# Kernel tuning notes

Measured on AMD Instinct MI355X. Metric: run time of the kernel, lower is better.

Reference implementation:

```python
import jax, jax.numpy as jnp
import numpy as np
import math

B, L, D = 4, 4096, 1024
D_EMB, D_HID = 3, 16


def make_pos_emb(emb_dim, seq_len):
    # Complex exponential positional embeddings (non-trainable), shape (1, seq_len, emb_dim)
    t = np.linspace(0.0, 1.0, seq_len, dtype=np.float32)[None, :, None]
    bands = (emb_dim - 1) // 2
    t_res = np.linspace(0.0, seq_len - 1, seq_len, dtype=np.float32)[None, :, None]
    w = 2.0 * math.pi * t_res / seq_len
    f = np.linspace(0.0001, max(bands - 1, 0), bands, dtype=np.float32)[None, None]
    z = np.exp(-1j * (f * w).astype(np.complex64))
    z = np.concatenate([t, z.real.astype(np.float32), z.imag.astype(np.float32)], axis=-1)
    return jnp.asarray(z)


def setup_inputs() -> dict:
    key = jax.random.key(0)
    ks = jax.random.split(key, 8)
    u = jax.random.normal(ks[0], (B, L, D), dtype=jnp.float32)
    z = make_pos_emb(D_EMB, L)  # (1, L, D_EMB)
    # filter MLP: Linear(d_emb, d_hidden) -> ReLU -> Linear(d_hidden, d_model)
    s1 = 1.0 / math.sqrt(D_EMB)
    w1 = jax.random.uniform(ks[1], (D_HID, D_EMB), jnp.float32, -s1, s1)
    b1 = jax.random.uniform(ks[2], (D_HID,), jnp.float32, -s1, s1)
    s2 = 1.0 / math.sqrt(D_HID)
    w2 = jax.random.uniform(ks[3], (D, D_HID), jnp.float32, -s2, s2)
    b2 = jax.random.uniform(ks[4], (D,), jnp.float32, -s2, s2)
    # projection: Linear(d_model, d_model)
    sp = 1.0 / math.sqrt(D)
    pw = jax.random.uniform(ks[5], (D, D), jnp.float32, -sp, sp)
    pb = jax.random.uniform(ks[6], (D,), jnp.float32, -sp, sp)
    return {"u": u, "z": z, "w1": w1, "b1": b1, "w2": w2, "b2": b2, "pw": pw, "pb": pb}


def fft_conv(u_bdl, k_dl):
    # u_bdl: (B, D, L), k_dl: (1, D, L) or (D, L)
    seqlen = u_bdl.shape[-1]
    fft_size = 2 * seqlen
    k_f = jnp.fft.rfft(k_dl, n=fft_size) / fft_size
    u_f = jnp.fft.rfft(u_bdl, n=fft_size)
    y = jnp.fft.irfft(u_f * k_f, n=fft_size, norm="forward")[..., :seqlen]
    return y


def reference(u, z, w1, b1, w2, b2, pw, pb):
    seqlen = u.shape[1]
    pe = z[:, :seqlen]  # (1, L, D_EMB)
    h = jax.nn.relu(jnp.einsum("ble,he->blh", pe, w1) + b1)
    filt = jnp.einsum("blh,dh->bld", h, w2) + b2  # (1, L, D)
    filt = jnp.transpose(filt, (0, 2, 1))  # (1, D, L)
    u_conv = fft_conv(jnp.transpose(u, (0, 2, 1)), filt)  # (B, D, L)
    u_conv = jnp.transpose(u_conv, (0, 2, 1)).astype(u.dtype)  # (B, L, D)
    u_proj = jnp.einsum("bld,od->blo", u, pw) + pb
    return u_conv * u_proj + u
```

## Files before the change

kernel.cpp:

```cpp
#include <hip/hip_runtime.h>
#include <hip/hip_bf16.h>

#define SEQL 4096
#define DCH  1024
#define BATCH 4

typedef __attribute__((ext_vector_type(2))) float cf;
__device__ __forceinline__ cf mkc(float x, float y){ cf r; r.x = x; r.y = y; return r; }
__device__ __forceinline__ cf cadd(cf a, cf b){ return a + b; }
__device__ __forceinline__ cf csub(cf a, cf b){ return a - b; }
__device__ __forceinline__ cf cmul(cf a, cf b){ return a.xx * b + mkc(-a.y, a.y) * b.yx; }
__device__ __forceinline__ cf cconjf(cf a){ return mkc(a.x, -a.y); }
__device__ __forceinline__ cf addi(cf a, cf b){ return a + mkc(-b.y, b.x); }
__device__ __forceinline__ cf subi(cf a, cf b){ return a - mkc(-b.y, b.x); }
__device__ __forceinline__ int phi(int c){ return c ^ ((c >> 4) & 15); }
__device__ __forceinline__ int drev(int i){
    return ((i>>10)&3) | (((i>>8)&3)<<2) | (((i>>6)&3)<<4)
         | (((i>>4)&3)<<6) | (((i>>2)&3)<<8) | ((i&3)<<10);
}

__device__ __forceinline__ cf W1c(int j){
    const float cs[4] = {1.f, 0.92387953f, 0.70710678f, 0.38268343f};
    const float sn[4] = {0.f, -0.38268343f, -0.70710678f, -0.92387953f};
    return mkc(cs[j], sn[j]);
}
__device__ __forceinline__ cf W2c(int j){
    const float cs[4] = {1.f, 0.70710678f, 0.f, -0.70710678f};
    const float sn[4] = {0.f, -0.70710678f, -1.f, -0.70710678f};
    return mkc(cs[j], sn[j]);
}
__device__ __forceinline__ cf W3c(int j){
    const float cs[4] = {1.f, 0.38268343f, -0.70710678f, -0.92387953f};
    const float sn[4] = {0.f, -0.92387953f, -0.70710678f, 0.38268343f};
    return mkc(cs[j], sn[j]);
}

__device__ __forceinline__ unsigned pack2bf(float a, float b){
    unsigned r;
    asm("v_cvt_pk_bf16_f32 %0, %1, %2" : "=v"(r) : "v"(a), "v"(b));
    return r;
}
__device__ __forceinline__ float bflo(unsigned u){ return __uint_as_float(u << 16); }
__device__ __forceinline__ float bfhi(unsigned u){ return __uint_as_float(u & 0xffff0000u); }

__device__ __forceinline__ void gload16(const void* g, void* l){
    __builtin_amdgcn_global_load_lds((const __attribute__((address_space(1))) void*)g,
                                     (__attribute__((address_space(3))) void*)l, 16, 0, 0);
}

__global__ __launch_bounds__(256) void prep_kernel(
        cf* __restrict__ tw4, cf* __restrict__ tw8, unsigned* __restrict__ idxt,
        const float* __restrict__ z, const float* __restrict__ w1,
        const float* __restrict__ b1, float* __restrict__ h,
        const float* __restrict__ pw, unsigned short* __restrict__ pwb) {
    const int blk = blockIdx.x;
    if (blk < 16) {
        int i = blk * 256 + threadIdx.x;
        const double TWO_PI = 6.283185307179586476925286766559;
        double a4 = -TWO_PI * (double)i / 4096.0;
        double a8 = -TWO_PI * (double)i / 8192.0;
        tw4[i] = mkc((float)cos(a4), (float)sin(a4));
        tw8[i] = mkc((float)cos(a8), (float)sin(a8));
    } else if (blk < 32) {
        int l = (blk - 16) * 256 + threadIdx.x;
        float pe0 = z[l * 3 + 0], pe1 = z[l * 3 + 1], pe2 = z[l * 3 + 2];
#pragma unroll
        for (int j = 0; j < 16; ++j) {
            float v = pe0 * w1[j * 3 + 0] + pe1 * w1[j * 3 + 1] + pe2 * w1[j * 3 + 2] + b1[j];
            h[l * 16 + j] = v > 0.f ? v : 0.f;
        }
    } else if (blk < 40) {
        int k = (blk - 32) * 256 + threadIdx.x;
        unsigned sk  = (unsigned)phi(drev(k));
        unsigned skk = (unsigned)phi(drev(4096 - k));
        idxt[k] = sk | (skk << 16);
    } else if (pwb) {
        int t = (blk - 40) * 256 + threadIdx.x;
        float4 a = *(const float4*)&pw[(size_t)t * 8];
        float4 b = *(const float4*)&pw[(size_t)t * 8 + 4];
        uint4 o;
        o.x = pack2bf(a.x, a.y); o.y = pack2bf(a.z, a.w);
        o.z = pack2bf(b.x, b.y); o.w = pack2bf(b.z, b.w);
        *(uint4*)&pwb[(size_t)t * 8] = o;
    }
}

__global__ __launch_bounds__(256) void transpose_kernel(
        const float* __restrict__ u, unsigned* __restrict__ utb,
        unsigned short* __restrict__ ub) {
    __shared__ float tile[32][33];
    int b = blockIdx.z;
    int l0 = blockIdx.x * 32;
    int d0 = blockIdx.y * 32;
    int tx = threadIdx.x, ty = threadIdx.y;
    const float* up = u + (size_t)b * SEQL * DCH;
    unsigned short* ubp = ub ? ub + (size_t)b * SEQL * DCH : (unsigned short*)0;
#pragma unroll
    for (int i = 0; i < 32; i += 8) {
        size_t idx = (size_t)(l0 + ty + i) * DCH + d0 + tx;
        float v = up[idx];
        tile[ty + i][tx] = v;
        if (ub) ubp[idx] = (unsigned short)pack2bf(v, v);
    }
    __syncthreads();
    unsigned* utp = utb + (size_t)b * DCH * (SEQL / 2);
    int t  = ty * 32 + tx;
    int dl = t >> 4;
    int lp = t & 15;
#pragma unroll
    for (int p = 0; p < 2; ++p) {
        int dd = dl + p * 16;
        unsigned v = pack2bf(tile[2 * lp][dd], tile[2 * lp + 1][dd]);
        utp[(size_t)(d0 + dd) * (SEQL / 2) + (l0 >> 1) + lp] = v;
    }
}

__device__ void dif_mid_and_chunk(cf* lds, const cf* __restrict__ tw){
    const int tid = threadIdx.x;
#pragma unroll
    for (int p = 1; p < 4; ++p) {
        const int lm = 10 - 2*p;
        const int m  = 1 << lm;
        const int step = 1024 >> lm;
#pragma unroll
        for (int it = 0; it < 4; ++it) {
            int j = tid + (it << 8);
            int k = j & (m-1);
            int g = j >> lm;
            int i0 = (g << (lm+2)) + k;
            cf x0 = lds[phi(i0)];
            cf x1 = lds[phi(i0+m)];
            cf x2 = lds[phi(i0+2*m)];
            cf x3 = lds[phi(i0+3*m)];
            cf b0 = cadd(x0,x2), b1 = csub(x0,x2);
            cf b2 = cadd(x1,x3), b3 = csub(x1,x3);
            cf u0 = cadd(b0,b2);
            cf u2 = csub(b0,b2);
            cf u1 = subi(b1,b3);
            cf u3 = addi(b1,b3);
            int t1 = k*step;
            lds[phi(i0)]     = u0;
            lds[phi(i0+m)]   = cmul(u1, tw[t1]);
            lds[phi(i0+2*m)] = cmul(u2, tw[2*t1]);
            lds[phi(i0+3*m)] = cmul(u3, tw[3*t1]);
        }
        __syncthreads();
    }
    {
        const int b0 = tid << 4;
        const int xr = tid & 15;
        cf v[16];
#pragma unroll
        for (int j=0;j<16;++j) v[j] = lds[b0 + (j ^ xr)];
#pragma unroll
        for (int j=0;j<4;++j){
            cf x0=v[j], x1=v[j+4], x2=v[j+8], x3=v[j+12];
            cf b0v=cadd(x0,x2), b1=csub(x0,x2), b2=cadd(x1,x3), b3=csub(x1,x3);
            cf u0=cadd(b0v,b2), u2=csub(b0v,b2), u1=subi(b1,b3), u3=addi(b1,b3);
            v[j]    = u0;
            v[j+4]  = cmul(u1, W1c(j));
            v[j+8]  = cmul(u2, W2c(j));
            v[j+12] = cmul(u3, W3c(j));
        }
#pragma unroll
        for (int c=0;c<4;++c){
            cf x0=v[4*c], x1=v[4*c+1], x2=v[4*c+2], x3=v[4*c+3];
            cf b0v=cadd(x0,x2), b1=csub(x0,x2), b2=cadd(x1,x3), b3=csub(x1,x3);
            v[4*c]   = cadd(b0v,b2);
            v[4*c+1] = subi(b1,b3);
            v[4*c+2] = csub(b0v,b2);
            v[4*c+3] = addi(b1,b3);
        }
#pragma unroll
        for (int j=0;j<16;++j) lds[b0 + (j ^ xr)] = v[j];
        __syncthreads();
    }
}

__device__ void dit_chunk_and_mid(cf* lds, const cf* __restrict__ tw){
    const int tid = threadIdx.x;
    {
        const int b0 = tid << 4;
        const int xr = tid & 15;
        cf v[16];
#pragma unroll
        for (int j=0;j<16;++j) v[j] = lds[b0 + (j ^ xr)];
#pragma unroll
        for (int c=0;c<4;++c){
            cf a0=v[4*c], a1=v[4*c+1], a2=v[4*c+2], a3=v[4*c+3];
            cf b0v=cadd(a0,a2), b1=csub(a0,a2), b2=cadd(a1,a3), b3=csub(a1,a3);
            v[4*c]   = cadd(b0v,b2);
            v[4*c+1] = addi(b1,b3);
            v[4*c+2] = csub(b0v,b2);
            v[4*c+3] = subi(b1,b3);
        }
#pragma unroll
        for (int j=0;j<4;++j){
            cf a0=v[j];
            cf a1=cmul(v[j+4],  cconjf(W1c(j)));
            cf a2=cmul(v[j+8],  cconjf(W2c(j)));
            cf a3=cmul(v[j+12], cconjf(W3c(j)));
            cf b0v=cadd(a0,a2), b1=csub(a0,a2), b2=cadd(a1,a3), b3=csub(a1,a3);
            v[j]    = cadd(b0v,b2);
            v[j+4]  = addi(b1,b3);
            v[j+8]  = csub(b0v,b2);
            v[j+12] = subi(b1,b3);
        }
#pragma unroll
        for (int j=0;j<16;++j) lds[b0 + (j ^ xr)] = v[j];
        __syncthreads();
    }
#pragma unroll
    for (int p = 0; p < 3; ++p) {
        const int lm = 4 + 2*p;
        const int m  = 1 << lm;
        const int step = 1024 >> lm;
#pragma unroll
        for (int it = 0; it < 4; ++it) {
            int j = tid + (it << 8);
            int k = j & (m-1);
            int g = j >> lm;
            int i0 = (g << (lm+2)) + k;
            int t1 = k*step;
            cf a0 = lds[phi(i0)];
            cf a1 = cmul(lds[phi(i0+m)],   cconjf(tw[t1]));
            cf a2 = cmul(lds[phi(i0+2*m)], cconjf(tw[2*t1]));
            cf a3 = cmul(lds[phi(i0+3*m)], cconjf(tw[3*t1]));
            cf b0=cadd(a0,a2), b1=csub(a0,a2), b2=cadd(a1,a3), b3=csub(a1,a3);
            lds[phi(i0)]     = cadd(b0,b2);
            lds[phi(i0+m)]   = addi(b1,b3);
            lds[phi(i0+2*m)] = csub(b0,b2);
            lds[phi(i0+3*m)] = subi(b1,b3);
        }
        __syncthreads();
    }
}

__global__ __launch_bounds__(256) void filt_fft_kernel(
        const float* __restrict__ h, const float* __restrict__ w2,
        const float* __restrict__ b2, const cf* __restrict__ tw4,
        const cf* __restrict__ tw8, cf* __restrict__ kfP,
        cf* __restrict__ kfP2, cf* __restrict__ kfQ) {
    __shared__ cf lds[4096];
    const int d = blockIdx.x;
    const int tid = threadIdx.x;
    float wv[16];
#pragma unroll
    for (int j = 0; j < 16; ++j) wv[j] = w2[d * 16 + j];
    const float bb = b2[d];
#pragma unroll
    for (int it = 0; it < 4; ++it) {
        int j = tid + (it << 8);
        const float* h0 = h + (size_t)(2*j) * 16;
        const float* h1 = h + (size_t)(2*(j+1024)) * 16;
        float f0 = bb, f1 = bb, f2 = bb, f3 = bb;
#pragma unroll
        for (int i = 0; i < 16; ++i) {
            f0 += h0[i] * wv[i];  f1 += h0[16+i] * wv[i];
            f2 += h1[i] * wv[i];  f3 += h1[16+i] * wv[i];
        }
        cf x0 = mkc(f0, f1), x1 = mkc(f2, f3);
        cf u0 = cadd(x0,x1);
        cf u2 = csub(x0,x1);
        cf u1 = subi(x0,x1);
        cf u3 = addi(x0,x1);
        lds[phi(j)]      = u0;
        lds[phi(j+1024)] = cmul(u1, tw4[j]);
        lds[phi(j+2048)] = cmul(u2, tw4[2*j]);
        lds[phi(j+3072)] = cmul(u3, tw4[3*j]);
    }
    __syncthreads();
    dif_mid_and_chunk(lds, tw4);
    const float s = 1.f / 8192.f;
    cf* Prow  = kfP  + (size_t)d * 2048;
    cf* P2row = kfP2 + (size_t)d * 2048;
    cf* Qrow  = kfQ  + (size_t)d * 2048;
    const int lane  = tid & 63;
    const int kbase = ((lane & 31) << 6) | ((lane >> 5) << 5) | ((tid >> 6) << 3);
#pragma unroll
    for (int it = 0; it < 8; ++it) {
        int k = kbase + it;
        if (k == 0) {
            cf c0 = lds[0];
            float H0 = (c0.x + c0.y) * s;
            float H4 = (c0.x - c0.y) * s;
            Prow[0]  = mkc(H0 + H4, H0 - H4);
            P2row[0] = mkc(H0 - H4, H0 + H4);
            cf c2 = lds[2];
            Qrow[0] = mkc(2.f * s * c2.x, 2.f * s * c2.y);
        } else {
            int kk = 4096 - k;
            cf ck  = lds[phi(drev(k))];
            cf ckk = lds[phi(drev(kk))];
            cf cc = cconjf(ckk);
            cf E  = (ck + cc) * 0.5f;
            cf Dd = csub(ck, cc);
            cf O  = mkc(Dd.y, -Dd.x) * 0.5f;
            cf wvv = tw8[k];
            cf Xk  = cadd(E, cmul(wvv, O));
            cf wp  = mkc(-wvv.x, wvv.y);
            cf Xkk = cadd(cconjf(E), cmul(wp, cconjf(O)));
            cf Hk  = Xk * s;
            cf Hkk = Xkk * s;
            float a = 1.f + wvv.y;
            float b = 1.f - wvv.y;
            cf Hkb = cconjf(Hkk);
            cf Hkc = cconjf(Hk);
            Prow[k]  = Hk * a + Hkb * b;
            P2row[k] = Hkk * a + Hkc * b;
            cf Qd = csub(Hk, Hkb);
            Qrow[k] = mkc(-Qd.y, Qd.x) * wvv.x;
        }
    }
}

__global__ __launch_bounds__(256) void conv_kernel(
        unsigned* __restrict__ utyb, const cf* __restrict__ tw4,
        const unsigned* __restrict__ idxt, const cf* __restrict__ kfP,
        const cf* __restrict__ kfP2, const cf* __restrict__ kfQ) {
    __shared__ cf lds[4096];
    const int row = blockIdx.x;
    const int d = row & (DCH - 1);
    const int tid = threadIdx.x;
    unsigned* rp = utyb + (size_t)row * (SEQL / 2);
#pragma unroll
    for (int it = 0; it < 4; ++it) {
        int j = tid + (it << 8);
        unsigned q0 = rp[j], q1 = rp[j + 1024];
        cf x0 = mkc(bflo(q0), bfhi(q0));
        cf x1 = mkc(bflo(q1), bfhi(q1));
        cf u0 = cadd(x0,x1);
        cf u2 = csub(x0,x1);
        cf u1 = subi(x0,x1);
        cf u3 = addi(x0,x1);
        lds[phi(j)]      = u0;
        lds[phi(j+1024)] = cmul(u1, tw4[j]);
        lds[phi(j+2048)] = cmul(u2, tw4[2*j]);
        lds[phi(j+3072)] = cmul(u3, tw4[3*j]);
    }
    __syncthreads();
    dif_mid_and_chunk(lds, tw4);
    const cf* Prow  = kfP  + (size_t)d * 2048;
    const cf* P2row = kfP2 + (size_t)d * 2048;
    const cf* Qrow  = kfQ  + (size_t)d * 2048;
    {
        const int lane  = tid & 63;
        const int kbase = ((lane & 31) << 6) | ((lane >> 5) << 5) | ((tid >> 6) << 3);
#pragma unroll
        for (int it = 0; it < 8; ++it) {
            int k = kbase + it;
            if (k == 0) {
                cf P0 = Prow[0], C0 = P2row[0], Q0 = Qrow[0];
                cf c0 = lds[0];
                lds[0] = P0 * c0.x + C0 * c0.y;
                cf c2 = lds[2];
                lds[2] = cmul(Q0, c2);
            } else {
                unsigned iv = idxt[k];
                int sk  = iv & 0xffff;
                int skk = iv >> 16;
                cf ck = lds[sk], ckk = lds[skk];
                cf Pv = Prow[k], P2v = P2row[k], Qv = Qrow[k];
                cf Zk  = cadd(cmul(Pv, ck),  cmul(Qv, cconjf(ckk)));
                cf Zkk = csub(cmul(P2v, ckk), cmul(cconjf(Qv), cconjf(ck)));
                lds[sk] = Zk; lds[skk] = Zkk;
            }
        }
    }
    __syncthreads();
    dit_chunk_and_mid(lds, tw4);
#pragma unroll
    for (int it = 0; it < 4; ++it) {
        int j = tid + (it << 8);
        cf a0 = lds[phi(j)];
        cf a1 = cmul(lds[phi(j+1024)], cconjf(tw4[j]));
        cf a2 = cmul(lds[phi(j+2048)], cconjf(tw4[2*j]));
        cf a3 = cmul(lds[phi(j+3072)], cconjf(tw4[3*j]));
        cf b0 = cadd(a0,a2), b1 = csub(a0,a2);
        cf b2 = cadd(a1,a3), b3 = csub(a1,a3);
        cf o0 = cadd(b0,b2);
        cf o1 = addi(b1,b3);
        rp[j]        = pack2bf(o0.x, o0.y);
        rp[j + 1024] = pack2bf(o1.x, o1.y);
    }
}

typedef __attribute__((ext_vector_type(8))) short short8;
typedef __attribute__((ext_vector_type(4))) float f32x4;

__global__ __launch_bounds__(512, 2) void gemm_mfma_v3(
        const unsigned short* __restrict__ ub, const unsigned short* __restrict__ pwb,
        const float* __restrict__ pb, const unsigned short* __restrict__ yb,
        float* __restrict__ out) {
    __shared__ char lds_raw[147456];
    float (*ysc)[132] = (float(*)[132])lds_raw;

    const int tid  = threadIdx.x;
    const int lane = tid & 63;
    const int wid  = tid >> 6;
    const int wr   = wid >> 1;
    const int wc   = wid & 1;
    const int m0   = blockIdx.x * 256;
    const int n0   = blockIdx.y * 128;

    f32x4 acc[4][4] = {};

#pragma unroll
    for (int tt = 0; tt < 2; ++tt) {
#pragma unroll
        for (int un = 0; un < 3; ++un) {
            const unsigned short* gs = (un == 2) ? pwb : ub;
            int growb = (un == 2) ? n0 : (m0 + un * 128);
#pragma unroll
            for (int j = 0; j < 2; ++j) {
                int rr = j * 64 + (tid >> 3);
                int ss = (tid & 7) ^ ((tid >> 3) & 7);
                gload16(gs + (size_t)(growb + rr) * 1024 + tt * 64 + ss * 8,
                        lds_raw + tt * 49152 + un * 16384 + rr * 128 + (tid & 7) * 16);
            }
        }
    }
    asm volatile("s_waitcnt vmcnt(6)" ::: "memory");
    __builtin_amdgcn_sched_barrier(0);
    __builtin_amdgcn_s_barrier();

    for (int t = 0; t < 16; ++t) {
        const int Ab  = (t % 3) * 49152;
        const int Bb  = Ab + 32768;
        const int sbB = ((t + 2) % 3) * 49152;
        const int kt2 = (t + 2) * 64;
#pragma unroll
        for (int q = 0; q < 4; ++q) {
            const int qr = q >> 1, qc = q & 1;
            short8 af[2][2], bfr[2][2];
#pragma unroll
            for (int f = 0; f < 2; ++f) {
                int arow = wr * 64 + qr * 32 + f * 16 + (lane & 15);
                int brow = wc * 64 + qc * 32 + f * 16 + (lane & 15);
#pragma unroll
                for (int kh = 0; kh < 2; ++kh) {
                    int ks = (lane >> 4) + 4 * kh;
                    af[f][kh]  = *(short8*)(lds_raw + Ab + arow * 128 + (ks ^ (arow & 7)) * 16);
                    bfr[f][kh] = *(short8*)(lds_raw + Bb + brow * 128 + (ks ^ (brow & 7)) * 16);
                }
            }
            if (q < 3 && t < 14) {
                const unsigned short* gs = (q == 2) ? pwb : ub;
                int growb = (q == 2) ? n0 : (m0 + q * 128);
#pragma unroll
                for (int j = 0; j < 2; ++j) {
                    int rr = j * 64 + (tid >> 3);
                    int ss = (tid & 7) ^ ((tid >> 3) & 7);
                    gload16(gs + (size_t)(growb + rr) * 1024 + kt2 + ss * 8,
                            lds_raw + sbB + q * 16384 + rr * 128 + (tid & 7) * 16);
                }
            }
            __builtin_amdgcn_s_barrier();
            asm volatile("s_waitcnt lgkmcnt(0)" ::: "memory");
            __builtin_amdgcn_sched_barrier(0);
            __builtin_amdgcn_s_setprio(1);
#pragma unroll
            for (int fa = 0; fa < 2; ++fa)
#pragma unroll
                for (int fb = 0; fb < 2; ++fb)
#pragma unroll
                    for (int kh = 0; kh < 2; ++kh)
                        acc[qr * 2 + fa][qc * 2 + fb] = __builtin_amdgcn_mfma_f32_16x16x32_bf16(
                            af[fa][kh], bfr[fb][kh], acc[qr * 2 + fa][qc * 2 + fb], 0, 0, 0);
            __builtin_amdgcn_s_setprio(0);
            if (q == 3) {
                if (t < 14)       asm volatile("s_waitcnt vmcnt(6)" ::: "memory");
                else if (t == 14) asm volatile("s_waitcnt vmcnt(0)" ::: "memory");
                __builtin_amdgcn_sched_barrier(0);
            }
            __builtin_amdgcn_s_barrier();
        }
    }

    __syncthreads();
    const int b  = m0 >> 12;
    const int l0 = m0 & (SEQL - 1);
    float pbv[4];
#pragma unroll
    for (int nf = 0; nf < 4; ++nf)
        pbv[nf] = pb[n0 + wc * 64 + nf * 16 + (lane & 15)];

    for (int c = 0; c < 2; ++c) {
        __syncthreads();
        {
            int dn = tid >> 2;
            int lq = tid & 3;
            const uint4* uptr = (const uint4*)(yb + (((size_t)(b * DCH + n0 + dn)) << 12) + l0 + c * 128);
#pragma unroll
            for (int jj = 0; jj < 4; ++jj) {
                uint4 w4 = uptr[lq * 4 + jj];
                int lb = (lq * 4 + jj) * 8;
                ysc[lb+0][dn] = bflo(w4.x); ysc[lb+1][dn] = bfhi(w4.x);
                ysc[lb+2][dn] = bflo(w4.y); ysc[lb+3][dn] = bfhi(w4.y);
                ysc[lb+4][dn] = bflo(w4.z); ysc[lb+5][dn] = bfhi(w4.z);
                ysc[lb+6][dn] = bflo(w4.w); ysc[lb+7][dn] = bfhi(w4.w);
            }
        }
        __syncthreads();
        if ((wr >> 1) == c) {
#pragma unroll
            for (int mf = 0; mf < 4; ++mf)
#pragma unroll
                for (int i = 0; i < 4; ++i) {
                    int lrow = (wr & 1) * 64 + mf * 16 + (lane >> 4) * 4 + i;
                    int m = m0 + c * 128 + lrow;
#pragma unroll
                    for (int nf = 0; nf < 4; ++nf) {
                        int nl = wc * 64 + nf * 16 + (lane & 15);
                        int n = n0 + nl;
                        float proj = acc[mf][nf][i] + pbv[nf];
                        float ures = __uint_as_float((unsigned)ub[(size_t)m * DCH + n] << 16);
                        out[(size_t)m * DCH + n] = ysc[lrow][nl] * proj + ures;
                    }
                }
        }
    }
}

__global__ __launch_bounds__(256, 3) void gemm_mfma_fb(
        const float* __restrict__ u, const float* __restrict__ pw,
        const float* __restrict__ pb, const unsigned short* __restrict__ yb,
        float* __restrict__ out) {
    __shared__ char lds_raw[34816];
    float (*ysc)[132] = (float(*)[132])lds_raw;
    const int tid  = threadIdx.x;
    const int lane = tid & 63;
    const int wid  = tid >> 6;
    const int wr   = wid >> 1;
    const int wc   = wid & 1;
    const int m0   = blockIdx.x * 128;
    const int n0   = blockIdx.y * 128;
    f32x4 acc[4][4] = {};
    float4 ra[4], rb[4];
    int s_row[4], s_f4[4];
#pragma unroll
    for (int j = 0; j < 4; ++j) {
        int idx = j * 256 + tid;
        s_row[j] = idx >> 3;
        s_f4[j]  = idx & 7;
    }
#define LOADT(kt)                                                                     \
    {                                                                                 \
        _Pragma("unroll")                                                             \
        for (int j = 0; j < 4; ++j) {                                                 \
            ra[j] = *(const float4*)&u [(size_t)(m0 + s_row[j]) * DCH + (kt) + s_f4[j] * 4]; \
            rb[j] = *(const float4*)&pw[(size_t)(n0 + s_row[j]) * DCH + (kt) + s_f4[j] * 4]; \
        }                                                                             \
    }
#define WRITET(base)                                                                  \
    {                                                                                 \
        _Pragma("unroll")                                                             \
        for (int j = 0; j < 4; ++j) {                                                 \
            int off = (base) + ((s_row[j] * 64 + s_f4[j] * 8) ^ ((s_row[j] & 3) << 4)); \
            uint2 pa, pbv2;                                                           \
            pa.x   = pack2bf(ra[j].x, ra[j].y);  pa.y   = pack2bf(ra[j].z, ra[j].w);  \
            pbv2.x = pack2bf(rb[j].x, rb[j].y);  pbv2.y = pack2bf(rb[j].z, rb[j].w);  \
            *(uint2*)(lds_raw + off)        = pa;                                     \
            *(uint2*)(lds_raw + off + 8192) = pbv2;                                   \
        }                                                                             \
    }
    LOADT(0);
    WRITET(0);
    LOADT(32);
    __syncthreads();
    for (int t = 0; t < 32; ++t) {
        const int cur = (t & 1) << 14;
        short8 af[4], bfr[4];
#pragma unroll
        for (int f = 0; f < 4; ++f) {
            int rowA = wr * 64 + f * 16 + (lane & 15);
            int rowB = wc * 64 + f * 16 + (lane & 15);
            int offA = cur + ((rowA * 64 + ((lane >> 4) * 16)) ^ ((rowA & 3) << 4));
            int offB = cur + 8192 + ((rowB * 64 + ((lane >> 4) * 16)) ^ ((rowB & 3) << 4));
            af[f]  = *(short8*)(lds_raw + offA);
            bfr[f] = *(short8*)(lds_raw + offB);
        }
        if (t < 31) WRITET(cur ^ 16384);
        if (t < 30) LOADT((t + 2) * 32);
#pragma unroll
        for (int mf = 0; mf < 4; ++mf)
#pragma unroll
            for (int nf = 0; nf < 4; ++nf)
                acc[mf][nf] = __builtin_amdgcn_mfma_f32_16x16x32_bf16(
                    af[mf], bfr[nf], acc[mf][nf], 0, 0, 0);
        __syncthreads();
    }
    const int b  = m0 >> 12;
    const int l0 = m0 & (SEQL - 1);
    float pbv[4];
#pragma unroll
    for (int nf = 0; nf < 4; ++nf)
        pbv[nf] = pb[n0 + wc * 64 + nf * 16 + (lane & 15)];
    for (int c = 0; c < 2; ++c) {
        __syncthreads();
#pragma unroll
        for (int j = 0; j < 4; ++j) {
            int idx = j * 256 + tid;
            int dn  = idx >> 3;
            int lg  = idx & 7;
            uint4 w4 = *(const uint4*)&yb[(((size_t)(b * DCH + n0 + dn)) << 12) + l0 + c * 64 + lg * 8];
            int lb = lg * 8;
            ysc[lb+0][dn] = bflo(w4.x); ysc[lb+1][dn] = bfhi(w4.x);
            ysc[lb+2][dn] = bflo(w4.y); ysc[lb+3][dn] = bfhi(w4.y);
            ysc[lb+4][dn] = bflo(w4.z); ysc[lb+5][dn] = bfhi(w4.z);
            ysc[lb+6][dn] = bflo(w4.w); ysc[lb+7][dn] = bfhi(w4.w);
        }
        __syncthreads();
        if (wr == c) {
#pragma unroll
            for (int mf = 0; mf < 4; ++mf)
#pragma unroll
                for (int i = 0; i < 4; ++i) {
                    int lrow = mf * 16 + (lane >> 4) * 4 + i;
                    int m = m0 + c * 64 + lrow;
#pragma unroll
                    for (int nf = 0; nf < 4; ++nf) {
                        int nl = wc * 64 + nf * 16 + (lane & 15);
                        int n = n0 + nl;
                        float proj = acc[mf][nf][i] + pbv[nf];
                        out[(size_t)m * DCH + n] = ysc[lrow][nl] * proj + u[(size_t)m * DCH + n];
                    }
                }
        }
    }
#undef LOADT
#undef WRITET
}

extern "C" void kernel_launch(void* const* d_in, const int* in_sizes, int n_in,
                              void* d_out, int out_size, void* d_ws, size_t ws_size,
                              hipStream_t stream) {
    const float* u  = (const float*)d_in[0];
    const float* z  = (const float*)d_in[1];
    const float* w1 = (const float*)d_in[2];
    const float* b1 = (const float*)d_in[3];
    const float* w2 = (const float*)d_in[4];
    const float* b2 = (const float*)d_in[5];
    const float* pw = (const float*)d_in[6];
    const float* pb = (const float*)d_in[7];
    float* out = (float*)d_out;

    float*    h    = (float*)d_ws;
    unsigned* utyb = (unsigned*)((char*)d_ws + 262144);

    cf* kfP  = (cf*)d_out;
    cf* kfP2 = (cf*)((char*)d_out + (16u << 20));
    cf* kfQ  = (cf*)((char*)d_out + (32u << 20));

    const size_t ub_off  = 262144 + (size_t)BATCH * DCH * (SEQL / 2) * sizeof(unsigned);
    const size_t pwb_off = ub_off + (size_t)BATCH * SEQL * DCH * sizeof(unsigned short);
    const size_t tw_off  = pwb_off + (size_t)DCH * DCH * sizeof(unsigned short);
    const size_t need    = tw_off + 2 * 4096 * sizeof(cf) + 2048 * sizeof(unsigned);
    const bool   big     = ws_size >= need;

    cf* tw4; unsigned* idxt;
    if (big) {
        tw4  = (cf*)((char*)d_ws + tw_off);
    } else {
        tw4  = (cf*)((char*)d_out + (56u << 20));
    }
    cf* tw8 = tw4 + 4096;
    idxt = (unsigned*)(tw8 + 4096);
    unsigned short* ub  = big ? (unsigned short*)((char*)d_ws + ub_off)  : (unsigned short*)0;
    unsigned short* pwb = big ? (unsigned short*)((char*)d_ws + pwb_off) : (unsigned short*)0;

    prep_kernel<<<dim3(big ? 552 : 40), dim3(256), 0, stream>>>(tw4, tw8, idxt, z, w1, b1, h, pw, pwb);
    transpose_kernel<<<dim3(SEQL / 32, DCH / 32, BATCH), dim3(32, 8), 0, stream>>>(u, utyb, ub);
    filt_fft_kernel<<<dim3(DCH), dim3(256), 0, stream>>>(h, w2, b2, tw4, tw8, kfP, kfP2, kfQ);
    conv_kernel<<<dim3(BATCH * DCH), dim3(256), 0, stream>>>(utyb, tw4, idxt, kfP, kfP2, kfQ);
    if (big)
        gemm_mfma_v3<<<dim3(64, 8), dim3(512), 0, stream>>>(ub, pwb, pb, (const unsigned short*)utyb, out);
    else
        gemm_mfma_fb<<<dim3(128, 8), dim3(256), 0, stream>>>(u, pw, pb, (const unsigned short*)utyb, out);
}
```

Measured before the change: 259.1 us.

## Run FFT conv and filter kernels with 512 threads and radix-4 stages

Doubles the block size of the filter FFT and convolution kernels from 256 to 512 threads. Each thread now does 2 instead of 4 radix-4 butterflies per stage. The in-register 16-point chunk is replaced by an extra LDS radix-4 stage plus an 8-element per-thread chunk. The aim is more parallelism per block and lower register pressure, so latency is hidden better. In exchange there is one more LDS pass and one more barrier per FFT direction.

```diff
diff --git a/kernel.cpp b/kernel.cpp
--- a/kernel.cpp
+++ b/kernel.cpp
@@ -17,22 +17,6 @@
 __device__ __forceinline__ int drev(int i){
     return ((i>>10)&3) | (((i>>8)&3)<<2) | (((i>>6)&3)<<4)
          | (((i>>4)&3)<<6) | (((i>>2)&3)<<8) | ((i&3)<<10);
-}
-
-__device__ __forceinline__ cf W1c(int j){
-    const float cs[4] = {1.f, 0.92387953f, 0.70710678f, 0.38268343f};
-    const float sn[4] = {0.f, -0.38268343f, -0.70710678f, -0.92387953f};
-    return mkc(cs[j], sn[j]);
-}
-__device__ __forceinline__ cf W2c(int j){
-    const float cs[4] = {1.f, 0.70710678f, 0.f, -0.70710678f};
-    const float sn[4] = {0.f, -0.70710678f, -1.f, -0.70710678f};
-    return mkc(cs[j], sn[j]);
-}
-__device__ __forceinline__ cf W3c(int j){
-    const float cs[4] = {1.f, 0.38268343f, -0.70710678f, -0.92387953f};
-    const float sn[4] = {0.f, -0.92387953f, -0.70710678f, 0.38268343f};
-    return mkc(cs[j], sn[j]);
 }
 
 __device__ __forceinline__ unsigned pack2bf(float a, float b){
@@ -115,16 +99,16 @@
     }
 }
 
-__device__ void dif_mid_and_chunk(cf* lds, const cf* __restrict__ tw){
+__device__ void dif_mid512(cf* lds, const cf* __restrict__ tw){
     const int tid = threadIdx.x;
 #pragma unroll
-    for (int p = 1; p < 4; ++p) {
-        const int lm = 10 - 2*p;
+    for (int p = 0; p < 4; ++p) {
+        const int lm = 8 - 2*p;
         const int m  = 1 << lm;
         const int step = 1024 >> lm;
 #pragma unroll
-        for (int it = 0; it < 4; ++it) {
-            int j = tid + (it << 8);
+        for (int it = 0; it < 2; ++it) {
+            int j = tid + (it << 9);
             int k = j & (m-1);
             int g = j >> lm;
             int i0 = (g << (lm+2)) + k;
@@ -134,90 +118,66 @@
             cf x3 = lds[phi(i0+3*m)];
             cf b0 = cadd(x0,x2), b1 = csub(x0,x2);
             cf b2 = cadd(x1,x3), b3 = csub(x1,x3);
-            cf u0 = cadd(b0,b2);
-            cf u2 = csub(b0,b2);
-            cf u1 = subi(b1,b3);
-            cf u3 = addi(b1,b3);
             int t1 = k*step;
-            lds[phi(i0)]     = u0;
-            lds[phi(i0+m)]   = cmul(u1, tw[t1]);
-            lds[phi(i0+2*m)] = cmul(u2, tw[2*t1]);
-            lds[phi(i0+3*m)] = cmul(u3, tw[3*t1]);
+            lds[phi(i0)]     = cadd(b0,b2);
+            lds[phi(i0+m)]   = cmul(subi(b1,b3), tw[t1]);
+            lds[phi(i0+2*m)] = cmul(csub(b0,b2), tw[2*t1]);
+            lds[phi(i0+3*m)] = cmul(addi(b1,b3), tw[3*t1]);
         }
         __syncthreads();
     }
     {
-        const int b0 = tid << 4;
-        const int xr = tid & 15;
-        cf v[16];
-#pragma unroll
-        for (int j=0;j<16;++j) v[j] = lds[b0 + (j ^ xr)];
-#pragma unroll
-        for (int j=0;j<4;++j){
-            cf x0=v[j], x1=v[j+4], x2=v[j+8], x3=v[j+12];
-            cf b0v=cadd(x0,x2), b1=csub(x0,x2), b2=cadd(x1,x3), b3=csub(x1,x3);
-            cf u0=cadd(b0v,b2), u2=csub(b0v,b2), u1=subi(b1,b3), u3=addi(b1,b3);
-            v[j]    = u0;
-            v[j+4]  = cmul(u1, W1c(j));
-            v[j+8]  = cmul(u2, W2c(j));
-            v[j+12] = cmul(u3, W3c(j));
-        }
-#pragma unroll
-        for (int c=0;c<4;++c){
-            cf x0=v[4*c], x1=v[4*c+1], x2=v[4*c+2], x3=v[4*c+3];
-            cf b0v=cadd(x0,x2), b1=csub(x0,x2), b2=cadd(x1,x3), b3=csub(x1,x3);
+        const int b0 = tid << 3;
+        const int xr = (b0 >> 4) & 15;
+        cf v[8];
+#pragma unroll
+        for (int e = 0; e < 8; ++e) v[e] = lds[(b0 + e) ^ xr];
+#pragma unroll
+        for (int c = 0; c < 2; ++c) {
+            cf x0 = v[4*c], x1 = v[4*c+1], x2 = v[4*c+2], x3 = v[4*c+3];
+            cf b0v = cadd(x0,x2), b1 = csub(x0,x2);
+            cf b2  = cadd(x1,x3), b3 = csub(x1,x3);
             v[4*c]   = cadd(b0v,b2);
             v[4*c+1] = subi(b1,b3);
             v[4*c+2] = csub(b0v,b2);
             v[4*c+3] = addi(b1,b3);
         }
 #pragma unroll
-        for (int j=0;j<16;++j) lds[b0 + (j ^ xr)] = v[j];
-        __syncthreads();
-    }
-}
-
-__device__ void dit_chunk_and_mid(cf* lds, const cf* __restrict__ tw){
+        for (int e = 0; e < 8; ++e) lds[(b0 + e) ^ xr] = v[e];
+        __syncthreads();
+    }
+}
+
+__device__ void dit_mid512(cf* lds, const cf* __restrict__ tw){
     const int tid = threadIdx.x;
     {
-        const int b0 = tid << 4;
-        const int xr = tid & 15;
-        cf v[16];
-#pragma unroll
-        for (int j=0;j<16;++j) v[j] = lds[b0 + (j ^ xr)];
-#pragma unroll
-        for (int c=0;c<4;++c){
-            cf a0=v[4*c], a1=v[4*c+1], a2=v[4*c+2], a3=v[4*c+3];
-            cf b0v=cadd(a0,a2), b1=csub(a0,a2), b2=cadd(a1,a3), b3=csub(a1,a3);
+        const int b0 = tid << 3;
+        const int xr = (b0 >> 4) & 15;
+        cf v[8];
+#pragma unroll
+        for (int e = 0; e < 8; ++e) v[e] = lds[(b0 + e) ^ xr];
+#pragma unroll
+        for (int c = 0; c < 2; ++c) {
+            cf a0 = v[4*c], a1 = v[4*c+1], a2 = v[4*c+2], a3 = v[4*c+3];
+            cf b0v = cadd(a0,a2), b1 = csub(a0,a2);
+            cf b2  = cadd(a1,a3), b3 = csub(a1,a3);
             v[4*c]   = cadd(b0v,b2);
             v[4*c+1] = addi(b1,b3);
             v[4*c+2] = csub(b0v,b2);
             v[4*c+3] = subi(b1,b3);
         }
 #pragma unroll
-        for (int j=0;j<4;++j){
-            cf a0=v[j];
-            cf a1=cmul(v[j+4],  cconjf(W1c(j)));
-            cf a2=cmul(v[j+8],  cconjf(W2c(j)));
-            cf a3=cmul(v[j+12], cconjf(W3c(j)));
-            cf b0v=cadd(a0,a2), b1=csub(a0,a2), b2=cadd(a1,a3), b3=csub(a1,a3);
-            v[j]    = cadd(b0v,b2);
-            v[j+4]  = addi(b1,b3);
-            v[j+8]  = csub(b0v,b2);
-            v[j+12] = subi(b1,b3);
-        }
-#pragma unroll
-        for (int j=0;j<16;++j) lds[b0 + (j ^ xr)] = v[j];
-        __syncthreads();
-    }
-#pragma unroll
-    for (int p = 0; p < 3; ++p) {
-        const int lm = 4 + 2*p;
+        for (int e = 0; e < 8; ++e) lds[(b0 + e) ^ xr] = v[e];
+        __syncthreads();
+    }
+#pragma unroll
+    for (int p = 0; p < 4; ++p) {
+        const int lm = 2 + 2*p;
         const int m  = 1 << lm;
         const int step = 1024 >> lm;
 #pragma unroll
-        for (int it = 0; it < 4; ++it) {
-            int j = tid + (it << 8);
+        for (int it = 0; it < 2; ++it) {
+            int j = tid + (it << 9);
             int k = j & (m-1);
             int g = j >> lm;
             int i0 = (g << (lm+2)) + k;
@@ -226,7 +186,8 @@
             cf a1 = cmul(lds[phi(i0+m)],   cconjf(tw[t1]));
             cf a2 = cmul(lds[phi(i0+2*m)], cconjf(tw[2*t1]));
             cf a3 = cmul(lds[phi(i0+3*m)], cconjf(tw[3*t1]));
-            cf b0=cadd(a0,a2), b1=csub(a0,a2), b2=cadd(a1,a3), b3=csub(a1,a3);
+            cf b0 = cadd(a0,a2), b1 = csub(a0,a2);
+            cf b2 = cadd(a1,a3), b3 = csub(a1,a3);
             lds[phi(i0)]     = cadd(b0,b2);
             lds[phi(i0+m)]   = addi(b1,b3);
             lds[phi(i0+2*m)] = csub(b0,b2);
@@ -236,7 +197,7 @@
     }
 }
 
-__global__ __launch_bounds__(256) void filt_fft_kernel(
+__global__ __launch_bounds__(512) void filt_fft_kernel(
         const float* __restrict__ h, const float* __restrict__ w2,
         const float* __restrict__ b2, const cf* __restrict__ tw4,
         const cf* __restrict__ tw8, cf* __restrict__ kfP,
@@ -249,8 +210,8 @@
     for (int j = 0; j < 16; ++j) wv[j] = w2[d * 16 + j];
     const float bb = b2[d];
 #pragma unroll
-    for (int it = 0; it < 4; ++it) {
-        int j = tid + (it << 8);
+    for (int it = 0; it < 2; ++it) {
+        int j = tid + (it << 9);
         const float* h0 = h + (size_t)(2*j) * 16;
         const float* h1 = h + (size_t)(2*(j+1024)) * 16;
         float f0 = bb, f1 = bb, f2 = bb, f3 = bb;
@@ -270,15 +231,16 @@
         lds[phi(j+3072)] = cmul(u3, tw4[3*j]);
     }
     __syncthreads();
-    dif_mid_and_chunk(lds, tw4);
+    dif_mid512(lds, tw4);
     const float s = 1.f / 8192.f;
     cf* Prow  = kfP  + (size_t)d * 2048;
     cf* P2row = kfP2 + (size_t)d * 2048;
     cf* Qrow  = kfQ  + (size_t)d * 2048;
     const int lane  = tid & 63;
-    const int kbase = ((lane & 31) << 6) | ((lane >> 5) << 5) | ((tid >> 6) << 3);
-#pragma unroll
-    for (int it = 0; it < 8; ++it) {
+    const int wid   = tid >> 6;
+    const int kbase = ((lane & 31) << 6) | ((lane >> 5) << 5) | (wid << 2);
+#pragma unroll
+    for (int it = 0; it < 4; ++it) {
         int k = kbase + it;
         if (k == 0) {
             cf c0 = lds[0];
@@ -314,7 +276,7 @@
     }
 }
 
-__global__ __launch_bounds__(256) void conv_kernel(
+__global__ __launch_bounds__(512) void conv_kernel(
         unsigned* __restrict__ utyb, const cf* __restrict__ tw4,
         const unsigned* __restrict__ idxt, const cf* __restrict__ kfP,
         const cf* __restrict__ kfP2, const cf* __restrict__ kfQ) {
@@ -324,8 +286,8 @@
     const int tid = threadIdx.x;
     unsigned* rp = utyb + (size_t)row * (SEQL / 2);
 #pragma unroll
-    for (int it = 0; it < 4; ++it) {
-        int j = tid + (it << 8);
+    for (int it = 0; it < 2; ++it) {
+        int j = tid + (it << 9);
         unsigned q0 = rp[j], q1 = rp[j + 1024];
         cf x0 = mkc(bflo(q0), bfhi(q0));
         cf x1 = mkc(bflo(q1), bfhi(q1));
@@ -339,15 +301,16 @@
         lds[phi(j+3072)] = cmul(u3, tw4[3*j]);
     }
     __syncthreads();
-    dif_mid_and_chunk(lds, tw4);
+    dif_mid512(lds, tw4);
     const cf* Prow  = kfP  + (size_t)d * 2048;
     const cf* P2row = kfP2 + (size_t)d * 2048;
     const cf* Qrow  = kfQ  + (size_t)d * 2048;
     {
         const int lane  = tid & 63;
-        const int kbase = ((lane & 31) << 6) | ((lane >> 5) << 5) | ((tid >> 6) << 3);
-#pragma unroll
-        for (int it = 0; it < 8; ++it) {
+        const int wid   = tid >> 6;
+        const int kbase = ((lane & 31) << 6) | ((lane >> 5) << 5) | (wid << 2);
+#pragma unroll
+        for (int it = 0; it < 4; ++it) {
             int k = kbase + it;
             if (k == 0) {
                 cf P0 = Prow[0], C0 = P2row[0], Q0 = Qrow[0];
@@ -368,10 +331,10 @@
         }
     }
     __syncthreads();
-    dit_chunk_and_mid(lds, tw4);
-#pragma unroll
-    for (int it = 0; it < 4; ++it) {
-        int j = tid + (it << 8);
+    dit_mid512(lds, tw4);
+#pragma unroll
+    for (int it = 0; it < 2; ++it) {
+        int j = tid + (it << 9);
         cf a0 = lds[phi(j)];
         cf a1 = cmul(lds[phi(j+1024)], cconjf(tw4[j]));
         cf a2 = cmul(lds[phi(j+2048)], cconjf(tw4[2*j]));
@@ -658,21 +621,21 @@
     const size_t need    = tw_off + 2 * 4096 * sizeof(cf) + 2048 * sizeof(unsigned);
     const bool   big     = ws_size >= need;
 
-    cf* tw4; unsigned* idxt;
+    cf* tw4;
     if (big) {
         tw4  = (cf*)((char*)d_ws + tw_off);
     } else {
         tw4  = (cf*)((char*)d_out + (56u << 20));
     }
     cf* tw8 = tw4 + 4096;
-    idxt = (unsigned*)(tw8 + 4096);
+    unsigned* idxt = (unsigned*)(tw8 + 4096);
     unsigned short* ub  = big ? (unsigned short*)((char*)d_ws + ub_off)  : (unsigned short*)0;
     unsigned short* pwb = big ? (unsigned short*)((char*)d_ws + pwb_off) : (unsigned short*)0;
 
     prep_kernel<<<dim3(big ? 552 : 40), dim3(256), 0, stream>>>(tw4, tw8, idxt, z, w1, b1, h, pw, pwb);
     transpose_kernel<<<dim3(SEQL / 32, DCH / 32, BATCH), dim3(32, 8), 0, stream>>>(u, utyb, ub);
-    filt_fft_kernel<<<dim3(DCH), dim3(256), 0, stream>>>(h, w2, b2, tw4, tw8, kfP, kfP2, kfQ);
-    conv_kernel<<<dim3(BATCH * DCH), dim3(256), 0, stream>>>(utyb, tw4, idxt, kfP, kfP2, kfQ);
+    filt_fft_kernel<<<dim3(DCH), dim3(512), 0, stream>>>(h, w2, b2, tw4, tw8, kfP, kfP2, kfQ);
+    conv_kernel<<<dim3(BATCH * DCH), dim3(512), 0, stream>>>(utyb, tw4, idxt, kfP, kfP2, kfQ);
     if (big)
         gemm_mfma_v3<<<dim3(64, 8), dim3(512), 0, stream>>>(ub, pwb, pb, (const unsigned short*)utyb, out);
     else
```

After: 310.1 us. +19.7%, slower.
